# Kernel tuning notes

Measured on AMD Instinct MI355X. Metric: run time of the kernel, lower is better.

## Reference

```python
import jax, jax.numpy as jnp
import numpy as np

B, T, F = 8, 512, 256
G, V = 2, 8192          # num_codebooks, num_embeddings per group
D = 16
DG = D // G             # per-group codevector dim = 8


def setup_inputs() -> dict:
    key = jax.random.key(0)
    k1, k2, k3, k4, k5 = jax.random.split(key, 5)
    x = jax.random.normal(k1, (B, T, F), dtype=jnp.float32)
    u = jax.random.uniform(k2, (B * T * G, V), dtype=jnp.float32)  # uniform for gumbel
    input_mask = jnp.ones((B, T), dtype=jnp.int32)
    embeddings = jax.random.uniform(k3, (1, G * V, DG), dtype=jnp.float32)
    W_proj = jax.random.normal(k4, (G * V, F), dtype=jnp.float32) * 0.02
    b_proj = jnp.zeros((G * V,), dtype=jnp.float32)
    return {"x": x, "u": u, "embeddings": embeddings,
            "W_proj": W_proj, "b_proj": b_proj, "input_mask": input_mask}


def reference(x, u, embeddings, W_proj, b_proj, input_mask):
    temperature = 1.0
    b, t, _ = x.shape
    # weight projection: [b, t, G*V]
    hidden = jnp.einsum("btf,gf->btg", x, W_proj) + b_proj
    h = hidden.reshape(b * t * G, V)
    # gumbel noise from uniform sample (matches torch.empty().uniform_(tiny, 1))
    tiny = jnp.finfo(h.dtype).tiny
    gumbels = -jnp.log(-jnp.log(jnp.clip(u, tiny, 1.0)))
    codevector_probs = jax.nn.softmax((h + gumbels) / temperature, axis=-1)  # [btG, V]
    # soft distribution (no noise) for perplexity
    soft = jax.nn.softmax(h.reshape(b * t, G, V), axis=-1)
    mask = input_mask.reshape(-1).astype(bool)  # [bt]
    masked = jnp.where(mask[:, None, None], soft, 0.0)
    marginal = masked.sum(0) / input_mask.sum().astype(soft.dtype)  # [G, V]
    perplexity = jnp.exp(-jnp.sum(marginal * jnp.log(marginal + 1e-7), axis=-1)).sum()
    targets_idx = jnp.argmax(codevector_probs, axis=-1).reshape(b, t, G)
    # per-group weighted codebook combination as GEMM (no huge broadcast intermediate)
    pg = codevector_probs.reshape(b * t, G, V)
    emb = embeddings.reshape(G, V, DG)
    codevectors = jnp.einsum("ngv,gvd->ngd", pg, emb).reshape(b, t, G * DG)
    return (codevectors, perplexity, targets_idx)
```

## Files before the change

kernel.cpp:

```cpp
#include <hip/hip_runtime.h>
#include <hip/hip_bf16.h>
#include <math.h>

#define Mrows 4096
#define Kdim  256
#define Ncols 16384
#define Vsz   8192
#define NSEG  16

typedef __attribute__((ext_vector_type(8))) short bf16x8;
typedef __attribute__((ext_vector_type(4))) float f32x4;

#define GLD16(ldsp, gp) __builtin_amdgcn_global_load_lds(                          \
    (const __attribute__((address_space(1))) unsigned int*)(gp),                   \
    (__attribute__((address_space(3))) unsigned int*)(ldsp), 16, 0, 0)

__global__ __launch_bounds__(256) void split_bf16(const float* __restrict__ src,
                                                  __hip_bfloat16* __restrict__ hi,
                                                  __hip_bfloat16* __restrict__ lo) {
    const int i = blockIdx.x * 256 + threadIdx.x;
    const float v = src[i];
    const __hip_bfloat16 h = __float2bfloat16(v);
    const float hf = __bfloat162float(h);
    hi[i] = h;
    lo[i] = __float2bfloat16(v - hf);
}

__global__ __launch_bounds__(256, 3) void gemm_mfma(const __hip_bfloat16* __restrict__ Ahi,
                                                    const __hip_bfloat16* __restrict__ Alo,
                                                    const __hip_bfloat16* __restrict__ Bhi,
                                                    const __hip_bfloat16* __restrict__ Blo,
                                                    const float* __restrict__ bias,
                                                    float* __restrict__ hid, int r0) {
    __shared__ unsigned short Ah[128 * 32], Al[128 * 32], Bh[128 * 32], Bl[128 * 32];
    const int tid = threadIdx.x;
    const int lane = tid & 63;
    const int wave = tid >> 6;

    const int gx = gridDim.x;
    int fid = blockIdx.y * gx + blockIdx.x;
    const int per = (gx * gridDim.y) >> 3;
    fid = (fid & 7) * per + (fid >> 3);
    const int bm = (fid % gx) * 128;
    const int bn = (fid / gx) * 128;

    const int wm = (wave & 1) * 64;
    const int wn = (wave >> 1) * 64;
    const int lm = lane & 15;
    const int sl = (((lane >> 4) ^ (lm & 3)) << 3);

    f32x4 acc[4][4];
#pragma unroll
    for (int i = 0; i < 4; ++i)
#pragma unroll
        for (int j = 0; j < 4; ++j) acc[i][j] = (f32x4){0.f, 0.f, 0.f, 0.f};

    for (int k0 = 0; k0 < Kdim; k0 += 32) {
        __syncthreads();
#pragma unroll
        for (int t = 0; t < 2; ++t) {
            const int c = tid + t * 256;
            const int row = c >> 2;
            const int ko = (((c & 3) ^ (row & 3)) << 3);
            const size_t ga = (size_t)(r0 + bm + row) * Kdim + k0 + ko;
            const size_t gb = (size_t)(bn + row) * Kdim + k0 + ko;
            GLD16(&Ah[c * 8], Ahi + ga);
            GLD16(&Al[c * 8], Alo + ga);
            GLD16(&Bh[c * 8], Bhi + gb);
            GLD16(&Bl[c * 8], Blo + gb);
        }
        __syncthreads();

        bf16x8 ah[4], al[4], bh[4], bl[4];
#pragma unroll
        for (int i = 0; i < 4; ++i) {
            ah[i] = *(const bf16x8*)&Ah[(wm + i * 16 + lm) * 32 + sl];
            al[i] = *(const bf16x8*)&Al[(wm + i * 16 + lm) * 32 + sl];
            bh[i] = *(const bf16x8*)&Bh[(wn + i * 16 + lm) * 32 + sl];
            bl[i] = *(const bf16x8*)&Bl[(wn + i * 16 + lm) * 32 + sl];
        }
#pragma unroll
        for (int j = 0; j < 4; ++j)
#pragma unroll
            for (int i = 0; i < 4; ++i)
                acc[i][j] = __builtin_amdgcn_mfma_f32_16x16x32_bf16(ah[i], bh[j], acc[i][j], 0, 0, 0);
#pragma unroll
        for (int j = 0; j < 4; ++j)
#pragma unroll
            for (int i = 0; i < 4; ++i)
                acc[i][j] = __builtin_amdgcn_mfma_f32_16x16x32_bf16(ah[i], bl[j], acc[i][j], 0, 0, 0);
#pragma unroll
        for (int j = 0; j < 4; ++j)
#pragma unroll
            for (int i = 0; i < 4; ++i)
                acc[i][j] = __builtin_amdgcn_mfma_f32_16x16x32_bf16(al[i], bh[j], acc[i][j], 0, 0, 0);
    }

    const int rbase = (lane >> 4) * 4;
#pragma unroll
    for (int j = 0; j < 4; ++j) {
        const int n = bn + wn + j * 16 + lm;
        const float bj = bias[n];
#pragma unroll
        for (int i = 0; i < 4; ++i) {
            const int m0 = bm + wm + i * 16 + rbase;
#pragma unroll
            for (int r2 = 0; r2 < 4; ++r2)
                hid[(size_t)(m0 + r2) * Ncols + n] = acc[i][j][r2] + bj;
        }
    }
}

__global__ __launch_bounds__(256, 4) void phase2(const float* __restrict__ hid,
                                                 const float* __restrict__ u,
                                                 const float* __restrict__ emb,
                                                 float* __restrict__ mrow,
                                                 float* __restrict__ out,
                                                 int r0) {
    const int tid = threadIdx.x;
    const int lane = tid & 63;
    const int wid = tid >> 6;
    const int n = r0 + blockIdx.x * 4 + wid;
    const int g = blockIdx.y;

    const float* hrow = hid + (size_t)(n - r0) * Ncols + (size_t)g * Vsz;
    const float* urow = u + ((size_t)n * 2 + g) * Vsz;
    const float* embg = emb + (size_t)g * Vsz * 8;

    float m1 = -INFINITY, s1 = 0.f, s2 = 0.f, bestl = -INFINITY;
    int besti = 0;
    float cv[8];
#pragma unroll
    for (int d2 = 0; d2 < 8; ++d2) cv[d2] = 0.f;

    float h0[8], u0[8], h1[8], u1[8];
#pragma unroll
    for (int k = 0; k < 8; ++k) {
        h0[k] = hrow[k * 64 + lane];
        u0[k] = __builtin_nontemporal_load(urow + k * 64 + lane);
    }

#define CHUNK(CH, CU, NH, NU, c) {                                                 \
    if ((c) + 1 < 16) {                                   \
        const int vb = ((c) + 1) * 512 + lane;                                     \
        _Pragma("unroll")                                                          \
        for (int k = 0; k < 8; ++k) {                                              \
            NH[k] = hrow[vb + k * 64];                                             \
            NU[k] = __builtin_nontemporal_load(urow + vb + k * 64);                \
        }                                                                          \
    }                                                                              \
    float l[8], inn[8];                                                            \
    float cmax = -INFINITY;                                                        \
    _Pragma("unroll")                                                              \
    for (int k = 0; k < 8; ++k) {                                                  \
        const float h = CH[k];                                                     \
        float uu = fminf(fmaxf(CU[k], 1.17549435e-38f), 1.0f);                     \
        const float d = uu - 1.0f;                                                 \
        float q = 1.0f / 9.0f;                                                     \
        q = fmaf(q, d, -0.125f);                                                   \
        q = fmaf(q, d, 1.0f / 7.0f);                                               \
        q = fmaf(q, d, -1.0f / 6.0f);                                              \
        q = fmaf(q, d, 0.2f);                                                      \
        q = fmaf(q, d, -0.25f);                                                    \
        q = fmaf(q, d, 1.0f / 3.0f);                                               \
        q = fmaf(q, d, -0.5f);                                                     \
        q = fmaf(q, d, 1.0f);                                                      \
        const float inner = (d > -0.2f) ? (-d) * q : -__logf(uu);                  \
        const float L = h - __logf(inner);                                         \
        l[k] = L; inn[k] = inner;                                                  \
        cmax = fmaxf(cmax, L);                                                     \
    }                                                                              \
    const float newm = fmaxf(m1, cmax);                                            \
    const float sc = __expf(m1 - newm);      \
    m1 = newm;                                                                     \
    s1 *= sc; s2 *= sc;                                                            \
    _Pragma("unroll")                                                              \
    for (int d2 = 0; d2 < 8; ++d2) cv[d2] *= sc;                                   \
    _Pragma("unroll")                                                              \
    for (int k = 0; k < 8; ++k) {                                                  \
        const float p = __expf(l[k] - m1);                                         \
        s1 += p;                                                                   \
        s2 = fmaf(p, inn[k], s2);                       \
        const int v = (c) * 512 + k * 64 + lane;                                   \
        const float4 e0 = *(const float4*)(embg + (size_t)v * 8);                  \
        const float4 e1 = *(const float4*)(embg + (size_t)v * 8 + 4);              \
        cv[0] = fmaf(p, e0.x, cv[0]); cv[1] = fmaf(p, e0.y, cv[1]);                \
        cv[2] = fmaf(p, e0.z, cv[2]); cv[3] = fmaf(p, e0.w, cv[3]);                \
        cv[4] = fmaf(p, e1.x, cv[4]); cv[5] = fmaf(p, e1.y, cv[5]);                \
        cv[6] = fmaf(p, e1.z, cv[6]); cv[7] = fmaf(p, e1.w, cv[7]);                \
        if (l[k] > bestl) { bestl = l[k]; besti = v; }                             \
    }                                                                              \
}

#pragma unroll
    for (int c = 0; c < 16; c += 2) {
        CHUNK(h0, u0, h1, u1, c)
        CHUNK(h1, u1, h0, u0, c + 1)
    }
#undef CHUNK

    float M = m1;
#pragma unroll
    for (int off = 32; off > 0; off >>= 1) M = fmaxf(M, __shfl_xor(M, off));
    const float scf = __expf(m1 - M);
    s1 *= scf; s2 *= scf;
#pragma unroll
    for (int d2 = 0; d2 < 8; ++d2) cv[d2] *= scf;
#pragma unroll
    for (int off = 32; off > 0; off >>= 1) {
        s1 += __shfl_xor(s1, off);
        s2 += __shfl_xor(s2, off);
    }
#pragma unroll
    for (int d2 = 0; d2 < 8; ++d2)
#pragma unroll
        for (int off = 32; off > 0; off >>= 1) cv[d2] += __shfl_xor(cv[d2], off);
#pragma unroll
    for (int off = 32; off > 0; off >>= 1) {
        const float ov = __shfl_xor(bestl, off);
        const int oi = __shfl_xor(besti, off);
        if (ov > bestl || (ov == bestl && oi < besti)) { bestl = ov; besti = oi; }
    }

    if (lane == 0) {
#pragma unroll
        for (int d2 = 0; d2 < 8; ++d2)
            out[(size_t)n * 16 + g * 8 + d2] = cv[d2] / s1;
        out[65537 + (size_t)n * 2 + g] = (float)besti;
        mrow[((size_t)n * 2 + g) * 2 + 0] = M;
        mrow[((size_t)n * 2 + g) * 2 + 1] = 1.0f / s2;
    }
}

__global__ __launch_bounds__(256) void marg_acc(const float* __restrict__ hid,
                                                const float* __restrict__ mrow,
                                                const int* __restrict__ mask,
                                                float* __restrict__ part) {
    const int v = blockIdx.x * 256 + threadIdx.x;
    const int seg = blockIdx.y;
    const int g = blockIdx.z;
    const float* hp = hid + (size_t)g * Vsz + v;
    const int nbeg = seg * (Mrows / NSEG);

    float a0 = 0.f, a1 = 0.f, a2 = 0.f, a3 = 0.f;
    for (int n = nbeg; n < nbeg + Mrows / NSEG; n += 4) {
#pragma unroll
        for (int q2 = 0; q2 < 4; ++q2) {
            const int nn = n + q2;
            const float M = mrow[((size_t)nn * 2 + g) * 2 + 0];
            const float is2 = mrow[((size_t)nn * 2 + g) * 2 + 1];
            const float sc = mask[nn] ? is2 : 0.f;
            const float e = __expf(hp[(size_t)nn * Ncols] - M);
            if (q2 == 0) a0 = fmaf(e, sc, a0);
            else if (q2 == 1) a1 = fmaf(e, sc, a1);
            else if (q2 == 2) a2 = fmaf(e, sc, a2);
            else a3 = fmaf(e, sc, a3);
        }
    }
    part[((size_t)seg * 2 + g) * Vsz + v] = (a0 + a1) + (a2 + a3);
}

__global__ __launch_bounds__(256) void reduce_marg(const float* __restrict__ part,
                                                   float* __restrict__ marginal) {
    const int g = blockIdx.y;
    const int v = blockIdx.x * 256 + threadIdx.x;
    float s = 0.f;
    for (int b = 0; b < NSEG; ++b) s += part[((size_t)b * 2 + g) * Vsz + v];
    marginal[g * Vsz + v] = s;
}

__global__ __launch_bounds__(256) void ppl_kernel(const float* __restrict__ marginal,
                                                  const int* __restrict__ mask,
                                                  float* __restrict__ out) {
    const int tid = threadIdx.x;
    const int lane = tid & 63;
    const int wid = tid >> 6;
    __shared__ float red[4];
    __shared__ int redi[4];

    int ms = 0;
    for (int i = tid; i < Mrows; i += 256) ms += mask[i];
#pragma unroll
    for (int off = 32; off > 0; off >>= 1) ms += __shfl_down(ms, off);
    if (lane == 0) redi[wid] = ms;
    __syncthreads();
    const float inv = 1.0f / (float)(redi[0] + redi[1] + redi[2] + redi[3]);

    float ppl = 0.f;
    for (int g = 0; g < 2; ++g) {
        float part = 0.f;
        for (int v = tid; v < Vsz; v += 256) {
            const float m = marginal[g * Vsz + v] * inv;
            part += m * logf(m + 1e-7f);
        }
#pragma unroll
        for (int off = 32; off > 0; off >>= 1) part += __shfl_down(part, off);
        __syncthreads();
        if (lane == 0) red[wid] = part;
        __syncthreads();
        if (tid == 0) ppl += __expf(-(red[0] + red[1] + red[2] + red[3]));
        __syncthreads();
    }
    if (tid == 0) out[65536] = ppl;
}

extern "C" void kernel_launch(void* const* d_in, const int* in_sizes, int n_in,
                              void* d_out, int out_size, void* d_ws, size_t ws_size,
                              hipStream_t stream) {
    const float* x    = (const float*)d_in[0];
    const float* u    = (const float*)d_in[1];
    const float* emb  = (const float*)d_in[2];
    const float* w    = (const float*)d_in[3];
    const float* bias = (const float*)d_in[4];
    const int*   mask = (const int*)d_in[5];
    float* out = (float*)d_out;

    char* base = (char*)d_ws;
    float* marginal = (float*)base;
    float* mrow = (float*)(base + 65536);
    float* part = (float*)(base + 131072);
    __hip_bfloat16* Ahi = (__hip_bfloat16*)(base + 1179648);
    __hip_bfloat16* Alo = Ahi + 1048576;
    __hip_bfloat16* Bhi = Alo + 1048576;
    __hip_bfloat16* Blo = Bhi + 4194304;
    const size_t hid_off = 1179648 + 4194304 + 16777216;
    float* hid = (float*)(base + hid_off);

    split_bf16<<<4096, 256, 0, stream>>>(x, Ahi, Alo);
    split_bf16<<<16384, 256, 0, stream>>>(w, Bhi, Blo);

    dim3 gg(Mrows / 128, Ncols / 128);
    gemm_mfma<<<gg, 256, 0, stream>>>(Ahi, Alo, Bhi, Blo, bias, hid, 0);
    dim3 pg(Mrows / 4, 2);
    phase2<<<pg, 256, 0, stream>>>(hid, u, emb, mrow, out, 0);

    marg_acc<<<dim3(Vsz / 256, NSEG, 2), 256, 0, stream>>>(hid, mrow, mask, part);
    reduce_marg<<<dim3(Vsz / 256, 2), 256, 0, stream>>>(part, marginal);
    ppl_kernel<<<1, 256, 0, stream>>>(marginal, mask, out);
}
```

Measured before the change: 725.6 us.

## Store exp(logits) from GEMM epilogue and drop online max in softmax passes

New measurement: 837.8 us. +15.5%, slower.

```diff
diff --git a/kernel.cpp b/kernel.cpp
--- a/kernel.cpp
+++ b/kernel.cpp
@@ -6,7 +6,7 @@
 #define Kdim  256
 #define Ncols 16384
 #define Vsz   8192
-#define NSEG  16
+#define NSEG  32
 
 typedef __attribute__((ext_vector_type(8))) short bf16x8;
 typedef __attribute__((ext_vector_type(4))) float f32x4;
@@ -31,7 +31,7 @@
                                                     const __hip_bfloat16* __restrict__ Bhi,
                                                     const __hip_bfloat16* __restrict__ Blo,
                                                     const float* __restrict__ bias,
-                                                    float* __restrict__ hid, int r0) {
+                                                    float* __restrict__ ehid) {
     __shared__ unsigned short Ah[128 * 32], Al[128 * 32], Bh[128 * 32], Bl[128 * 32];
     const int tid = threadIdx.x;
     const int lane = tid & 63;
@@ -62,7 +62,7 @@
             const int c = tid + t * 256;
             const int row = c >> 2;
             const int ko = (((c & 3) ^ (row & 3)) << 3);
-            const size_t ga = (size_t)(r0 + bm + row) * Kdim + k0 + ko;
+            const size_t ga = (size_t)(bm + row) * Kdim + k0 + ko;
             const size_t gb = (size_t)(bn + row) * Kdim + k0 + ko;
             GLD16(&Ah[c * 8], Ahi + ga);
             GLD16(&Al[c * 8], Alo + ga);
@@ -106,158 +106,159 @@
             const int m0 = bm + wm + i * 16 + rbase;
 #pragma unroll
             for (int r2 = 0; r2 < 4; ++r2)
-                hid[(size_t)(m0 + r2) * Ncols + n] = acc[i][j][r2] + bj;
-        }
-    }
-}
-
-__global__ __launch_bounds__(256, 4) void phase2(const float* __restrict__ hid,
+                ehid[(size_t)(m0 + r2) * Ncols + n] = __expf(acc[i][j][r2] + bj);
+        }
+    }
+}
+
+#define GUMRATIO(EH, UU, ROUT) {                                                   \
+    float uu = fminf(fmaxf((UU), 1.17549435e-38f), 1.0f);                          \
+    const float d = uu - 1.0f;                                                     \
+    float q = 1.0f / 9.0f;                                                         \
+    q = fmaf(q, d, -0.125f);                                                       \
+    q = fmaf(q, d, 1.0f / 7.0f);                                                   \
+    q = fmaf(q, d, -1.0f / 6.0f);                                                  \
+    q = fmaf(q, d, 0.2f);                                                          \
+    q = fmaf(q, d, -0.25f);                                                        \
+    q = fmaf(q, d, 1.0f / 3.0f);                                                   \
+    q = fmaf(q, d, -0.5f);                                                         \
+    q = fmaf(q, d, 1.0f);                                                          \
+    const float inner = (d > -0.2f) ? (-d) * q : -__logf(uu);                      \
+    ROUT = (EH) * __builtin_amdgcn_rcpf(inner); }
+
+__global__ __launch_bounds__(256, 4) void phase2(const float* __restrict__ ehid,
                                                  const float* __restrict__ u,
                                                  const float* __restrict__ emb,
+                                                 const int* __restrict__ mask,
                                                  float* __restrict__ mrow,
-                                                 float* __restrict__ out,
-                                                 int r0) {
+                                                 float* __restrict__ out) {
     const int tid = threadIdx.x;
     const int lane = tid & 63;
     const int wid = tid >> 6;
-    const int n = r0 + blockIdx.x * 4 + wid;
+    const int n = blockIdx.x * 8 + wid * 2;
     const int g = blockIdx.y;
 
-    const float* hrow = hid + (size_t)(n - r0) * Ncols + (size_t)g * Vsz;
-    const float* urow = u + ((size_t)n * 2 + g) * Vsz;
+    const float* ha = ehid + (size_t)n * Ncols + (size_t)g * Vsz;
+    const float* hb = ha + Ncols;
+    const float* ua = u + ((size_t)n * 2 + g) * Vsz;
+    const float* ub = ua + 2 * Vsz;
     const float* embg = emb + (size_t)g * Vsz * 8;
-
-    float m1 = -INFINITY, s1 = 0.f, s2 = 0.f, bestl = -INFINITY;
-    int besti = 0;
-    float cv[8];
-#pragma unroll
-    for (int d2 = 0; d2 < 8; ++d2) cv[d2] = 0.f;
-
-    float h0[8], u0[8], h1[8], u1[8];
-#pragma unroll
-    for (int k = 0; k < 8; ++k) {
-        h0[k] = hrow[k * 64 + lane];
-        u0[k] = __builtin_nontemporal_load(urow + k * 64 + lane);
-    }
-
-#define CHUNK(CH, CU, NH, NU, c) {                                                 \
-    if ((c) + 1 < 16) {                                   \
-        const int vb = ((c) + 1) * 512 + lane;                                     \
+    const int mka = mask[n], mkb = mask[n + 1];
+
+    float s1a = 0.f, s2a = 0.f, s1b = 0.f, s2b = 0.f;
+    float bra = -1.f, brb = -1.f;
+    int bia = 0, bib = 0;
+    float cva[8], cvb[8];
+#pragma unroll
+    for (int d2 = 0; d2 < 8; ++d2) { cva[d2] = 0.f; cvb[d2] = 0.f; }
+
+    float HA0[4], UA0[4], HB0[4], UB0[4], HA1[4], UA1[4], HB1[4], UB1[4];
+#pragma unroll
+    for (int k = 0; k < 4; ++k) {
+        const int v = k * 64 + lane;
+        HA0[k] = ha[v]; UA0[k] = __builtin_nontemporal_load(ua + v);
+        HB0[k] = hb[v]; UB0[k] = __builtin_nontemporal_load(ub + v);
+    }
+
+#define CHUNK(CHA, CUA, CHB, CUB, NHA, NUA, NHB, NUB, c) {                         \
+    if ((c) + 1 < 32) {                                   \
+        const int vb = ((c) + 1) * 256 + lane;                                     \
         _Pragma("unroll")                                                          \
-        for (int k = 0; k < 8; ++k) {                                              \
-            NH[k] = hrow[vb + k * 64];                                             \
-            NU[k] = __builtin_nontemporal_load(urow + vb + k * 64);                \
+        for (int k = 0; k < 4; ++k) {                                              \
+            NHA[k] = ha[vb + k * 64];                                              \
+            NUA[k] = __builtin_nontemporal_load(ua + vb + k * 64);                 \
+            NHB[k] = hb[vb + k * 64];                                              \
+            NUB[k] = __builtin_nontemporal_load(ub + vb + k * 64);                 \
         }                                                                          \
     }                                                                              \
-    float l[8], inn[8];                                                            \
-    float cmax = -INFINITY;                                                        \
     _Pragma("unroll")                                                              \
-    for (int k = 0; k < 8; ++k) {                                                  \
-        const float h = CH[k];                                                     \
-        float uu = fminf(fmaxf(CU[k], 1.17549435e-38f), 1.0f);                     \
-        const float d = uu - 1.0f;                                                 \
-        float q = 1.0f / 9.0f;                                                     \
-        q = fmaf(q, d, -0.125f);                                                   \
-        q = fmaf(q, d, 1.0f / 7.0f);                                               \
-        q = fmaf(q, d, -1.0f / 6.0f);                                              \
-        q = fmaf(q, d, 0.2f);                                                      \
-        q = fmaf(q, d, -0.25f);                                                    \
-        q = fmaf(q, d, 1.0f / 3.0f);                                               \
-        q = fmaf(q, d, -0.5f);                                                     \
-        q = fmaf(q, d, 1.0f);                                                      \
-        const float inner = (d > -0.2f) ? (-d) * q : -__logf(uu);                  \
-        const float L = h - __logf(inner);                                         \
-        l[k] = L; inn[k] = inner;                                                  \
-        cmax = fmaxf(cmax, L);                                                     \
-    }                                                                              \
-    const float newm = fmaxf(m1, cmax);                                            \
-    const float sc = __expf(m1 - newm);      \
-    m1 = newm;                                                                     \
-    s1 *= sc; s2 *= sc;                                                            \
-    _Pragma("unroll")                                                              \
-    for (int d2 = 0; d2 < 8; ++d2) cv[d2] *= sc;                                   \
-    _Pragma("unroll")                                                              \
-    for (int k = 0; k < 8; ++k) {                                                  \
-        const float p = __expf(l[k] - m1);                                         \
-        s1 += p;                                                                   \
-        s2 = fmaf(p, inn[k], s2);                       \
-        const int v = (c) * 512 + k * 64 + lane;                                   \
+    for (int k = 0; k < 4; ++k) {                                                  \
+        const int v = (c) * 256 + k * 64 + lane;                                   \
+        float ra, rb;                                                              \
+        GUMRATIO(CHA[k], CUA[k], ra)                                               \
+        GUMRATIO(CHB[k], CUB[k], rb)                                               \
+        s1a += ra; s2a += CHA[k];                                                  \
+        s1b += rb; s2b += CHB[k];                                                  \
+        if (ra > bra) { bra = ra; bia = v; }                                       \
+        if (rb > brb) { brb = rb; bib = v; }                                       \
         const float4 e0 = *(const float4*)(embg + (size_t)v * 8);                  \
         const float4 e1 = *(const float4*)(embg + (size_t)v * 8 + 4);              \
-        cv[0] = fmaf(p, e0.x, cv[0]); cv[1] = fmaf(p, e0.y, cv[1]);                \
-        cv[2] = fmaf(p, e0.z, cv[2]); cv[3] = fmaf(p, e0.w, cv[3]);                \
-        cv[4] = fmaf(p, e1.x, cv[4]); cv[5] = fmaf(p, e1.y, cv[5]);                \
-        cv[6] = fmaf(p, e1.z, cv[6]); cv[7] = fmaf(p, e1.w, cv[7]);                \
-        if (l[k] > bestl) { bestl = l[k]; besti = v; }                             \
+        cva[0] = fmaf(ra, e0.x, cva[0]); cva[1] = fmaf(ra, e0.y, cva[1]);          \
+        cva[2] = fmaf(ra, e0.z, cva[2]); cva[3] = fmaf(ra, e0.w, cva[3]);          \
+        cva[4] = fmaf(ra, e1.x, cva[4]); cva[5] = fmaf(ra, e1.y, cva[5]);          \
+        cva[6] = fmaf(ra, e1.z, cva[6]); cva[7] = fmaf(ra, e1.w, cva[7]);          \
+        cvb[0] = fmaf(rb, e0.x, cvb[0]); cvb[1] = fmaf(rb, e0.y, cvb[1]);          \
+        cvb[2] = fmaf(rb, e0.z, cvb[2]); cvb[3] = fmaf(rb, e0.w, cvb[3]);          \
+        cvb[4] = fmaf(rb, e1.x, cvb[4]); cvb[5] = fmaf(rb, e1.y, cvb[5]);          \
+        cvb[6] = fmaf(rb, e1.z, cvb[6]); cvb[7] = fmaf(rb, e1.w, cvb[7]);          \
     }                                                                              \
 }
 
 #pragma unroll
-    for (int c = 0; c < 16; c += 2) {
-        CHUNK(h0, u0, h1, u1, c)
-        CHUNK(h1, u1, h0, u0, c + 1)
+    for (int c = 0; c < 32; c += 2) {
+        CHUNK(HA0, UA0, HB0, UB0, HA1, UA1, HB1, UB1, c)
+        CHUNK(HA1, UA1, HB1, UB1, HA0, UA0, HB0, UB0, c + 1)
     }
 #undef CHUNK
 
-    float M = m1;
-#pragma unroll
-    for (int off = 32; off > 0; off >>= 1) M = fmaxf(M, __shfl_xor(M, off));
-    const float scf = __expf(m1 - M);
-    s1 *= scf; s2 *= scf;
-#pragma unroll
-    for (int d2 = 0; d2 < 8; ++d2) cv[d2] *= scf;
 #pragma unroll
     for (int off = 32; off > 0; off >>= 1) {
-        s1 += __shfl_xor(s1, off);
-        s2 += __shfl_xor(s2, off);
+        s1a += __shfl_xor(s1a, off); s2a += __shfl_xor(s2a, off);
+        s1b += __shfl_xor(s1b, off); s2b += __shfl_xor(s2b, off);
     }
 #pragma unroll
     for (int d2 = 0; d2 < 8; ++d2)
 #pragma unroll
-        for (int off = 32; off > 0; off >>= 1) cv[d2] += __shfl_xor(cv[d2], off);
+        for (int off = 32; off > 0; off >>= 1) {
+            cva[d2] += __shfl_xor(cva[d2], off);
+            cvb[d2] += __shfl_xor(cvb[d2], off);
+        }
 #pragma unroll
     for (int off = 32; off > 0; off >>= 1) {
-        const float ov = __shfl_xor(bestl, off);
-        const int oi = __shfl_xor(besti, off);
-        if (ov > bestl || (ov == bestl && oi < besti)) { bestl = ov; besti = oi; }
+        const float ova = __shfl_xor(bra, off);
+        const int oia = __shfl_xor(bia, off);
+        if (ova > bra || (ova == bra && oia < bia)) { bra = ova; bia = oia; }
+        const float ovb = __shfl_xor(brb, off);
+        const int oib = __shfl_xor(bib, off);
+        if (ovb > brb || (ovb == brb && oib < bib)) { brb = ovb; bib = oib; }
     }
 
     if (lane == 0) {
 #pragma unroll
-        for (int d2 = 0; d2 < 8; ++d2)
-            out[(size_t)n * 16 + g * 8 + d2] = cv[d2] / s1;
-        out[65537 + (size_t)n * 2 + g] = (float)besti;
-        mrow[((size_t)n * 2 + g) * 2 + 0] = M;
-        mrow[((size_t)n * 2 + g) * 2 + 1] = 1.0f / s2;
-    }
-}
-
-__global__ __launch_bounds__(256) void marg_acc(const float* __restrict__ hid,
+        for (int d2 = 0; d2 < 8; ++d2) {
+            out[(size_t)n * 16 + g * 8 + d2] = cva[d2] / s1a;
+            out[(size_t)(n + 1) * 16 + g * 8 + d2] = cvb[d2] / s1b;
+        }
+        out[65537 + (size_t)n * 2 + g] = (float)bia;
+        out[65537 + (size_t)(n + 1) * 2 + g] = (float)bib;
+        mrow[n * 2 + g] = mka ? (1.0f / s2a) : 0.f;
+        mrow[(n + 1) * 2 + g] = mkb ? (1.0f / s2b) : 0.f;
+    }
+}
+
+__global__ __launch_bounds__(256) void marg_acc(const float* __restrict__ ehid,
                                                 const float* __restrict__ mrow,
-                                                const int* __restrict__ mask,
                                                 float* __restrict__ part) {
-    const int v = blockIdx.x * 256 + threadIdx.x;
+    const int v4 = (blockIdx.x * 256 + threadIdx.x) * 4;
     const int seg = blockIdx.y;
     const int g = blockIdx.z;
-    const float* hp = hid + (size_t)g * Vsz + v;
+    const float* hp = ehid + (size_t)g * Vsz + v4;
     const int nbeg = seg * (Mrows / NSEG);
 
-    float a0 = 0.f, a1 = 0.f, a2 = 0.f, a3 = 0.f;
-    for (int n = nbeg; n < nbeg + Mrows / NSEG; n += 4) {
-#pragma unroll
-        for (int q2 = 0; q2 < 4; ++q2) {
-            const int nn = n + q2;
-            const float M = mrow[((size_t)nn * 2 + g) * 2 + 0];
-            const float is2 = mrow[((size_t)nn * 2 + g) * 2 + 1];
-            const float sc = mask[nn] ? is2 : 0.f;
-            const float e = __expf(hp[(size_t)nn * Ncols] - M);
-            if (q2 == 0) a0 = fmaf(e, sc, a0);
-            else if (q2 == 1) a1 = fmaf(e, sc, a1);
-            else if (q2 == 2) a2 = fmaf(e, sc, a2);
-            else a3 = fmaf(e, sc, a3);
-        }
-    }
-    part[((size_t)seg * 2 + g) * Vsz + v] = (a0 + a1) + (a2 + a3);
+    float4 a0 = {0.f, 0.f, 0.f, 0.f}, a1 = {0.f, 0.f, 0.f, 0.f};
+    for (int nn = nbeg; nn < nbeg + Mrows / NSEG; nn += 2) {
+        const float4 e0 = *(const float4*)(hp + (size_t)nn * Ncols);
+        const float4 e1 = *(const float4*)(hp + (size_t)(nn + 1) * Ncols);
+        const float w0 = mrow[nn * 2 + g];
+        const float w1 = mrow[(nn + 1) * 2 + g];
+        a0.x = fmaf(e0.x, w0, a0.x); a0.y = fmaf(e0.y, w0, a0.y);
+        a0.z = fmaf(e0.z, w0, a0.z); a0.w = fmaf(e0.w, w0, a0.w);
+        a1.x = fmaf(e1.x, w1, a1.x); a1.y = fmaf(e1.y, w1, a1.y);
+        a1.z = fmaf(e1.z, w1, a1.z); a1.w = fmaf(e1.w, w1, a1.w);
+    }
+    float4 r;
+    r.x = a0.x + a1.x; r.y = a0.y + a1.y; r.z = a0.z + a1.z; r.w = a0.w + a1.w;
+    *(float4*)(part + ((size_t)seg * 2 + g) * Vsz + v4) = r;
 }
 
 __global__ __launch_bounds__(256) void reduce_marg(const float* __restrict__ part,
@@ -319,22 +320,22 @@
     float* marginal = (float*)base;
     float* mrow = (float*)(base + 65536);
     float* part = (float*)(base + 131072);
-    __hip_bfloat16* Ahi = (__hip_bfloat16*)(base + 1179648);
+    __hip_bfloat16* Ahi = (__hip_bfloat16*)(base + 2228224);
     __hip_bfloat16* Alo = Ahi + 1048576;
     __hip_bfloat16* Bhi = Alo + 1048576;
     __hip_bfloat16* Blo = Bhi + 4194304;
-    const size_t hid_off = 1179648 + 4194304 + 16777216;
-    float* hid = (float*)(base + hid_off);
+    const size_t ehid_off = 2228224 + 4194304 + 16777216;
+    float* ehid = (float*)(base + ehid_off);
 
     split_bf16<<<4096, 256, 0, stream>>>(x, Ahi, Alo);
     split_bf16<<<16384, 256, 0, stream>>>(w, Bhi, Blo);
 
     dim3 gg(Mrows / 128, Ncols / 128);
-    gemm_mfma<<<gg, 256, 0, stream>>>(Ahi, Alo, Bhi, Blo, bias, hid, 0);
-    dim3 pg(Mrows / 4, 2);
-    phase2<<<pg, 256, 0, stream>>>(hid, u, emb, mrow, out, 0);
-
-    marg_acc<<<dim3(Vsz / 256, NSEG, 2), 256, 0, stream>>>(hid, mrow, mask, part);
+    gemm_mfma<<<gg, 256, 0, stream>>>(Ahi, Alo, Bhi, Blo, bias, ehid);
+    dim3 pg(Mrows / 8, 2);
+    phase2<<<pg, 256, 0, stream>>>(ehid, u, emb, mask, mrow, out);
+
+    marg_acc<<<dim3(Vsz / 1024, NSEG, 2), 256, 0, stream>>>(ehid, mrow, part);
     reduce_marg<<<dim3(Vsz / 256, 2), 256, 0, stream>>>(part, marginal);
     ppl_kernel<<<1, 256, 0, stream>>>(marginal, mask, out);
 }
```
